# Performance work log

Hardware: AMD Instinct MI355X
Metric: run time of the kernel (lower is better)

Reference implementation:

```python
import jax, jax.numpy as jnp
import numpy as np

MAX_K_QK = 64
MAX_K_V = 64
MAX_K_KNOW = 128


def threshold_gate(scores, tau, max_k):
    # scores: [B,S,N], tau: [B,S,1]
    raw = scores - tau
    gate = jnp.where(raw > 0, raw, 1e-08 * jnp.exp(raw))
    exp_gate = jnp.exp(gate) - 1.0
    k = min(max_k, scores.shape[-1])
    topk_vals, _ = jax.lax.top_k(exp_gate, k)
    threshold = topk_vals[:, :, -1:]
    exp_gate = jnp.where(exp_gate >= threshold, exp_gate, 0.0)
    gate_sum = exp_gate.sum(axis=-1, keepdims=True) + 1e-08
    gate_strength = jnp.tanh(exp_gate.max(axis=-1, keepdims=True))
    return exp_gate / gate_sum * gate_strength


def setup_inputs() -> dict:
    key = jax.random.key(0)
    ks = jax.random.split(key, 8)
    B, S, D = 2, 2048, 1024
    N_QK, N_V, N_KNOW = 4096, 4096, 8192
    scale = 0.02  # keep scores in a sane range for exp()
    return {
        "x": jax.random.normal(ks[0], (B, S, D), jnp.float32),
        "qk_emb": jax.random.normal(ks[1], (N_QK, D), jnp.float32) * scale,
        "v_emb": jax.random.normal(ks[2], (N_V, D), jnp.float32) * scale,
        "know_emb": jax.random.normal(ks[3], (N_KNOW, D), jnp.float32) * scale,
        "w_attn": jax.random.normal(ks[4], (D, 3), jnp.float32) * scale,
        "b_attn": jnp.zeros((3,), jnp.float32),
        "w_know": jax.random.normal(ks[5], (D, 1), jnp.float32) * scale,
        "b_know": jnp.zeros((1,), jnp.float32),
    }


def reference(x, qk_emb, v_emb, know_emb, w_attn, b_attn, w_know, b_know):
    # deterministic=True -> router dropout is identity
    # attention gates
    scores_qk = jnp.einsum("bsd,nd->bsn", x, qk_emb)
    scores_v = jnp.einsum("bsd,nd->bsn", x, v_emb)
    tau_all = x @ w_attn + b_attn  # [B,S,3]
    g_Q = threshold_gate(scores_qk, tau_all[:, :, 0:1], MAX_K_QK)
    g_K = threshold_gate(scores_qk, tau_all[:, :, 1:2], MAX_K_QK)
    g_V = threshold_gate(scores_v, tau_all[:, :, 2:3], MAX_K_V)
    t_qk = 1.0 / qk_emb.shape[0]
    t_v = 1.0 / v_emb.shape[0]
    aux_attn = (
        ((g_Q.mean(axis=(0, 1)) - t_qk) ** 2).sum() * g_Q.shape[-1]
        + ((g_K.mean(axis=(0, 1)) - t_qk) ** 2).sum() * g_K.shape[-1]
        + ((g_V.mean(axis=(0, 1)) - t_v) ** 2).sum() * g_V.shape[-1]
    )
    # knowledge gates
    scores_know = jnp.einsum("bsd,nd->bsn", x, know_emb)
    tau_know = x @ w_know + b_know  # [B,S,1]
    g_know = threshold_gate(scores_know, tau_know, MAX_K_KNOW)
    t_know = 1.0 / know_emb.shape[0]
    aux_know = ((g_know.mean(axis=(0, 1)) - t_know) ** 2).sum() * g_know.shape[-1]
    return (g_Q, g_K, g_V, aux_attn, g_know, aux_know)
```

## Files before the change

### kernel.cpp

```cpp
#include <hip/hip_runtime.h>
#include <hip/hip_bf16.h>


#define M_ROWS 4096
#define DIM    1024
#define N_QK   4096
#define N_KNOW 8192

typedef unsigned short ushortT;
typedef __attribute__((ext_vector_type(8)))  short short8;
typedef __attribute__((ext_vector_type(16))) float f32x16;

__global__ __launch_bounds__(256) void tau_kernel(
    const float* __restrict__ x, const float* __restrict__ w_attn,
    const float* __restrict__ b_attn, const float* __restrict__ w_know,
    const float* __restrict__ b_know, float* __restrict__ tau4, int D)
{
    __shared__ float s_f[4][4];
    const int row = blockIdx.x;
    const int tid = threadIdx.x;
    const float* xr = x + (size_t)row * D;
    float p0 = 0.f, p1 = 0.f, p2 = 0.f, p3 = 0.f;
    for (int d = tid; d < D; d += 256) {
        float xv = xr[d];
        p0 += xv * w_attn[d * 3 + 0];
        p1 += xv * w_attn[d * 3 + 1];
        p2 += xv * w_attn[d * 3 + 2];
        p3 += xv * w_know[d];
    }
#pragma unroll
    for (int o = 32; o > 0; o >>= 1) {
        p0 += __shfl_down(p0, o, 64);
        p1 += __shfl_down(p1, o, 64);
        p2 += __shfl_down(p2, o, 64);
        p3 += __shfl_down(p3, o, 64);
    }
    const int lane = tid & 63, wv = tid >> 6;
    if (lane == 0) { s_f[wv][0] = p0; s_f[wv][1] = p1; s_f[wv][2] = p2; s_f[wv][3] = p3; }
    __syncthreads();
    if (tid < 4) {
        float v = s_f[0][tid] + s_f[1][tid] + s_f[2][tid] + s_f[3][tid];
        v += (tid < 3) ? b_attn[tid] : b_know[0];
        tau4[(size_t)row * 4 + tid] = v;
    }
}

__device__ __forceinline__ void split4(const float4 v, uint2& H, uint2& L) {
    float vv[4] = {v.x, v.y, v.z, v.w};
    unsigned h[4], l[4];
#pragma unroll
    for (int i = 0; i < 4; i++) {
        __hip_bfloat16 hb = __float2bfloat16(vv[i]);
        float r = vv[i] - __bfloat162float(hb);
        __hip_bfloat16 lb = __float2bfloat16(r);
        h[i] = *(ushortT*)&hb;
        l[i] = *(ushortT*)&lb;
    }
    H.x = h[0] | (h[1] << 16); H.y = h[2] | (h[3] << 16);
    L.x = l[0] | (l[1] << 16); L.y = l[2] | (l[3] << 16);
}

__global__ __launch_bounds__(256) void convertA(
    const float* __restrict__ src, ushortT* __restrict__ dst, int nElem4)
{
    int g = blockIdx.x * 256 + threadIdx.x;
    if (g >= nElem4) return;
    int row = g >> 8;
    int c4  = g & 255;
    int chunk = c4 >> 3, pos = c4 & 7;
    const float4 v = *(const float4*)(src + (size_t)row * DIM + c4 * 4);
    uint2 H, L;
    split4(v, H, L);
    ushortT* base = dst + (size_t)row * 2048 + chunk * 64;
    *(uint2*)(base + pos * 4)      = H;
    *(uint2*)(base + 32 + pos * 4) = L;
}

__global__ __launch_bounds__(256) void gemm_fused3(
    const ushortT* __restrict__ Aext, const ushortT* __restrict__ Bext,
    float* __restrict__ gQ, float* __restrict__ gV, float* __restrict__ gKn,
    int nb0)
{
    __shared__ ushortT AHL[2][128 * 64];
    __shared__ ushortT BHL[2][128 * 64];
    const int tid = threadIdx.x;
    const int wave = tid >> 6, lane = tid & 63;
    const int l32 = lane & 31, h = lane >> 5;
    const int rx7 = l32 & 7;
    const int wm = (wave >> 1) * 64, wn = (wave & 1) * 64;
    const long long m0 = (long long)blockIdx.y * 128;
    const int nblk = nb0 + blockIdx.x;

    float* C; long long ldc; long long n0;
    if (nblk < 32)      { C = gQ;  ldc = N_QK;   n0 = (long long)nblk * 128; }
    else if (nblk < 64) { C = gV;  ldc = N_QK;   n0 = (long long)(nblk - 32) * 128; }
    else                { C = gKn; ldc = N_KNOW; n0 = (long long)(nblk - 64) * 128; }

    const ushortT* gAp[4]; const ushortT* gBp[4]; int lOff[4];
#pragma unroll
    for (int it = 0; it < 4; ++it) {
        int f = it * 256 + tid;
        int r = f >> 3, sp = f & 7;
        int sg = sp ^ (r & 7);
        gAp[it] = Aext + (m0 + r) * 2048 + sg * 8;
        gBp[it] = Bext + ((long long)blockIdx.x * 128 + r) * 2048 + sg * 8;
        lOff[it] = f * 8;
    }

    f32x16 acc[2][2] = {};

#define STAGE(buf, c) do {                                                         \
    _Pragma("unroll")                                                              \
    for (int it = 0; it < 4; ++it) {                                               \
        __builtin_amdgcn_global_load_lds(                                          \
            (const __attribute__((address_space(1))) unsigned*)(const void*)(gAp[it] + (c) * 64), \
            (__attribute__((address_space(3))) unsigned*)(void*)(&AHL[buf][0] + lOff[it]), 16, 0, 0); \
        __builtin_amdgcn_global_load_lds(                                          \
            (const __attribute__((address_space(1))) unsigned*)(const void*)(gBp[it] + (c) * 64), \
            (__attribute__((address_space(3))) unsigned*)(void*)(&BHL[buf][0] + lOff[it]), 16, 0, 0); \
    }                                                                              \
} while (0)

#define COMPUTE(buf) do {                                                          \
    _Pragma("unroll")                                                              \
    for (int kb = 0; kb < 2; ++kb) {                                               \
        const int so = ((kb * 2 + h) ^ rx7) * 16;                                  \
        short8 aH[2], aL[2], bH[2], bL[2];                                         \
        _Pragma("unroll")                                                          \
        for (int t = 0; t < 2; ++t) {                                              \
            const char* pa = (const char*)(&AHL[buf][0]) + (wm + t * 32 + l32) * 128; \
            const char* pb = (const char*)(&BHL[buf][0]) + (wn + t * 32 + l32) * 128; \
            aH[t] = *(const short8*)(pa + so);                                     \
            aL[t] = *(const short8*)(pa + (so ^ 64));                              \
            bH[t] = *(const short8*)(pb + so);                                     \
            bL[t] = *(const short8*)(pb + (so ^ 64));                              \
        }                                                                          \
        _Pragma("unroll")                                                          \
        for (int i = 0; i < 2; ++i)                                                \
            _Pragma("unroll")                                                      \
            for (int j = 0; j < 2; ++j) {                                          \
                acc[i][j] = __builtin_amdgcn_mfma_f32_32x32x16_bf16(aH[i], bH[j], acc[i][j], 0, 0, 0); \
                acc[i][j] = __builtin_amdgcn_mfma_f32_32x32x16_bf16(aH[i], bL[j], acc[i][j], 0, 0, 0); \
                acc[i][j] = __builtin_amdgcn_mfma_f32_32x32x16_bf16(aL[i], bH[j], acc[i][j], 0, 0, 0); \
                acc[i][j] = __builtin_amdgcn_mfma_f32_32x32x16_bf16(aL[i], bL[j], acc[i][j], 0, 0, 0); \
            }                                                                      \
    }                                                                              \
} while (0)

    STAGE(0, 0);
    __syncthreads();

    for (int c = 0; c < 32; c += 2) {
        STAGE(1, c + 1);
        COMPUTE(0);
        __syncthreads();
        if (c + 2 < 32) STAGE(0, c + 2);
        COMPUTE(1);
        __syncthreads();
    }
#undef STAGE
#undef COMPUTE

#pragma unroll
    for (int ti = 0; ti < 2; ++ti)
#pragma unroll
        for (int tj = 0; tj < 2; ++tj) {
            long long col = n0 + wn + tj * 32 + l32;
            long long rb  = m0 + wm + ti * 32 + 4 * h;
#pragma unroll
            for (int reg = 0; reg < 16; ++reg) {
                long long row = rb + (reg & 3) + 8 * (reg >> 2);
                C[row * ldc + col] = acc[ti][tj][reg];
            }
        }
}

__global__ __launch_bounds__(256) void gemm_fused2(
    const ushortT* __restrict__ Aext, const float* __restrict__ qk_emb,
    const float* __restrict__ v_emb, const float* __restrict__ know_emb,
    float* __restrict__ gQ, float* __restrict__ gV, float* __restrict__ gKn,
    long long rowOff)
{
    __shared__ ushortT AHL[128 * 64];
    __shared__ ushortT BHL[128 * 64];
    const int tid = threadIdx.x;
    const int wave = tid >> 6, lane = tid & 63;
    const int l32 = lane & 31, h = lane >> 5;
    const int rx7 = l32 & 7;
    const int wm = (wave >> 1) * 64, wn = (wave & 1) * 64;
    const long long m0 = (long long)blockIdx.y * 128;
    const int nblk = blockIdx.x;

    const float* Bsrc; float* C; long long ldc; long long n0;
    if (nblk < 32)      { Bsrc = qk_emb;   C = gQ;  ldc = N_QK;   n0 = (long long)nblk * 128; }
    else if (nblk < 64) { Bsrc = v_emb;    C = gV;  ldc = N_QK;   n0 = (long long)(nblk - 32) * 128; }
    else                { Bsrc = know_emb; C = gKn; ldc = N_KNOW; n0 = (long long)(nblk - 64) * 128; }

    const ushortT* gAp[4]; ushortT* lAp[4];
    const float*   gBp[4]; int offH[4], offL[4];
#pragma unroll
    for (int it = 0; it < 4; ++it) {
        int f = it * 256 + tid;
        int r = f >> 3, sp = f & 7;
        int sg = sp ^ (r & 7);
        gAp[it] = Aext + (m0 + r) * 2048 + sg * 8;
        lAp[it] = AHL + f * 8;
        int c4 = f & 7;
        int s = c4 >> 1, hf = c4 & 1;
        offH[it] = r * 128 + ((s ^ (r & 7)) * 16) + hf * 8;
        offL[it] = r * 128 + (((4 | s) ^ (r & 7)) * 16) + hf * 8;
        gBp[it] = Bsrc + (n0 + r) * DIM + c4 * 4;
    }
    const char* pA[2]; const char* pB[2];
#pragma unroll
    for (int t = 0; t < 2; ++t) {
        pA[t] = (const char*)AHL + (wm + t * 32 + l32) * 128;
        pB[t] = (const char*)BHL + (wn + t * 32 + l32) * 128;
    }

    f32x16 acc[2][2] = {};
    float4 bufB[4];
#pragma unroll
    for (int it = 0; it < 4; ++it) bufB[it] = *(const float4*)(gBp[it]);

    for (int c = 0; c < 32; ++c) {
#pragma unroll
        for (int it = 0; it < 4; ++it) {
            __builtin_amdgcn_global_load_lds(
                (const __attribute__((address_space(1))) unsigned*)(const void*)(gAp[it] + c * 64),
                (__attribute__((address_space(3))) unsigned*)(void*)lAp[it], 16, 0, 0);
            uint2 H, L;
            split4(bufB[it], H, L);
            *(uint2*)((char*)BHL + offH[it]) = H;
            *(uint2*)((char*)BHL + offL[it]) = L;
        }
        __syncthreads();
        if (c + 1 < 32) {
#pragma unroll
            for (int it = 0; it < 4; ++it)
                bufB[it] = *(const float4*)(gBp[it] + (c + 1) * 32);
        }
#pragma unroll
        for (int kb = 0; kb < 2; ++kb) {
            const int so = ((kb * 2 + h) ^ rx7) * 16;
            short8 aH[2], aL[2], bH[2], bL[2];
#pragma unroll
            for (int t = 0; t < 2; ++t) {
                aH[t] = *(const short8*)(pA[t] + so);
                aL[t] = *(const short8*)(pA[t] + (so ^ 64));
                bH[t] = *(const short8*)(pB[t] + so);
                bL[t] = *(const short8*)(pB[t] + (so ^ 64));
            }
#pragma unroll
            for (int i = 0; i < 2; ++i)
#pragma unroll
                for (int j = 0; j < 2; ++j) {
                    acc[i][j] = __builtin_amdgcn_mfma_f32_32x32x16_bf16(aH[i], bH[j], acc[i][j], 0, 0, 0);
                    acc[i][j] = __builtin_amdgcn_mfma_f32_32x32x16_bf16(aH[i], bL[j], acc[i][j], 0, 0, 0);
                    acc[i][j] = __builtin_amdgcn_mfma_f32_32x32x16_bf16(aL[i], bH[j], acc[i][j], 0, 0, 0);
                    acc[i][j] = __builtin_amdgcn_mfma_f32_32x32x16_bf16(aL[i], bL[j], acc[i][j], 0, 0, 0);
                }
        }
        __syncthreads();
    }
#pragma unroll
    for (int ti = 0; ti < 2; ++ti)
#pragma unroll
        for (int tj = 0; tj < 2; ++tj) {
            long long col = n0 + wn + tj * 32 + l32;
            long long rb  = rowOff + m0 + wm + ti * 32 + 4 * h;
#pragma unroll
            for (int reg = 0; reg < 16; ++reg) {
                long long row = rb + (reg & 3) + 8 * (reg >> 2);
                C[row * ldc + col] = acc[ti][tj][reg];
            }
        }
}

__device__ __forceinline__ unsigned floatToKey(float f) {
    unsigned b = __float_as_uint(f);
    return (b & 0x80000000u) ? ~b : (b | 0x80000000u);
}
__device__ __forceinline__ float keyToFloat(unsigned key) {
    unsigned b = (key & 0x80000000u) ? (key & 0x7FFFFFFFu) : ~key;
    return __uint_as_float(b);
}
__device__ __forceinline__ float egate(float raw) {
    float g = raw > 0.f ? raw : 1e-8f * __expf(raw);
    return expf(g) - 1.f;
}

template <int NV, bool VLOAD, bool VSTORE>
__device__ __forceinline__ void gate_body(
    const float* __restrict__ srow, float tA, float tB, bool hasB, int ksel,
    float* __restrict__ orowA, float* __restrict__ orowB,
    float* __restrict__ colA, float* __restrict__ colB,
    int* s_cnt, unsigned* s_u, float* s_f)
{
    const int tid = threadIdx.x, lane = tid & 63, wv = tid >> 6;

    unsigned keys[NV * 4];
    unsigned kmax = 0u;
#pragma unroll
    for (int i = 0; i < NV; i++) {
        float v0, v1, v2, v3;
        if (VLOAD) {
            float4 v = *(const float4*)(srow + (size_t)(i * 256 + tid) * 4);
            v0 = v.x; v1 = v.y; v2 = v.z; v3 = v.w;
        } else {
            v0 = srow[(i * 4 + 0) * 256 + tid];
            v1 = srow[(i * 4 + 1) * 256 + tid];
            v2 = srow[(i * 4 + 2) * 256 + tid];
            v3 = srow[(i * 4 + 3) * 256 + tid];
        }
        unsigned a = floatToKey(v0), b = floatToKey(v1);
        unsigned c = floatToKey(v2), d = floatToKey(v3);
        keys[i * 4 + 0] = a; keys[i * 4 + 1] = b;
        keys[i * 4 + 2] = c; keys[i * 4 + 3] = d;
        unsigned m1 = a > b ? a : b, m2 = c > d ? c : d;
        m1 = m1 > m2 ? m1 : m2;
        kmax = kmax > m1 ? kmax : m1;
    }
#pragma unroll
    for (int o = 32; o > 0; o >>= 1) {
        unsigned x = __shfl_down(kmax, o, 64);
        kmax = kmax > x ? kmax : x;
    }
    if (lane == 0) s_u[wv] = kmax;
    __syncthreads();
    { unsigned a = s_u[0], b = s_u[1], c = s_u[2], d = s_u[3];
      unsigned m1 = a > b ? a : b, m2 = c > d ? c : d; kmax = m1 > m2 ? m1 : m2; }

    unsigned lo = 0u, hi = kmax, vk;
    int pp = 0;
    for (;;) {
        if (lo >= hi) { vk = lo; break; }
        unsigned mid = lo + ((hi - lo + 1u) >> 1);
        int c = 0;
#pragma unroll
        for (int i = 0; i < NV * 4; i++) c += (keys[i] >= mid) ? 1 : 0;
#pragma unroll
        for (int o = 32; o > 0; o >>= 1) c += __shfl_down(c, o, 64);
        if (lane == 0) s_cnt[pp * 4 + wv] = c;
        __syncthreads();
        int total = s_cnt[pp * 4 + 0] + s_cnt[pp * 4 + 1]
                  + s_cnt[pp * 4 + 2] + s_cnt[pp * 4 + 3];
        pp ^= 1;
        if (total == ksel) { vk = mid; break; }
        if (total > ksel) lo = mid; else hi = mid - 1u;
    }

    float sA = 0.f, sB = 0.f;
#pragma unroll
    for (int i = 0; i < NV * 4; i++) {
        if (keys[i] >= vk) {
            float s = keyToFloat(keys[i]);
            sA += egate(s - tA);
            if (hasB) sB += egate(s - tB);
        }
    }
#pragma unroll
    for (int o = 32; o > 0; o >>= 1) {
        sA += __shfl_down(sA, o, 64);
        sB += __shfl_down(sB, o, 64);
    }
    if (lane == 0) { s_f[wv] = sA; s_f[4 + wv] = sB; }
    __syncthreads();
    sA = s_f[0] + s_f[1] + s_f[2] + s_f[3];
    sB = s_f[4] + s_f[5] + s_f[6] + s_f[7];

    const float smax = keyToFloat(kmax);
    const float scaleA = tanhf(egate(smax - tA)) / (sA + 1e-8f);
    const float scaleB = hasB ? tanhf(egate(smax - tB)) / (sB + 1e-8f) : 0.f;

#pragma unroll
    for (int i = 0; i < NV; i++) {
        float ga[4], gb[4];
        int eidx[4];
#pragma unroll
        for (int j = 0; j < 4; j++) {
            int ii = i * 4 + j;
            int idx = VLOAD ? (i * 1024 + tid * 4 + j) : (ii * 256 + tid);
            eidx[j] = idx;
            unsigned key = keys[ii];
            float vA = 0.f, vB = 0.f;
            if (key >= vk) {
                float s = keyToFloat(key);
                vA = egate(s - tA) * scaleA;
                atomicAdd(&colA[idx], vA);
                if (hasB) { vB = egate(s - tB) * scaleB; atomicAdd(&colB[idx], vB); }
            }
            ga[j] = vA; gb[j] = vB;
        }
        if (VSTORE) {
            *(float4*)(orowA + (size_t)eidx[0]) = make_float4(ga[0], ga[1], ga[2], ga[3]);
            if (hasB) *(float4*)(orowB + (size_t)eidx[0]) = make_float4(gb[0], gb[1], gb[2], gb[3]);
        } else {
#pragma unroll
            for (int j = 0; j < 4; j++) {
                orowA[eidx[j]] = ga[j];
                if (hasB) orowB[eidx[j]] = gb[j];
            }
        }
    }
}

__global__ __launch_bounds__(256) void gate_all(
    const float* __restrict__ tau4,
    float* __restrict__ gQ, float* __restrict__ gK,
    float* __restrict__ gV, float* __restrict__ gKn,
    float* __restrict__ colsums)
{
    __shared__ int s_cnt[8];
    __shared__ unsigned s_u[4];
    __shared__ float s_f[8];
    const int bid = blockIdx.x;
    if (bid < 4096) {
        const int row = bid;
        const float t = tau4[(size_t)row * 4 + 3];
        gate_body<8, false, false>(
            gKn + (size_t)row * N_KNOW, t, 0.f, false, 128,
            gKn + (size_t)row * N_KNOW, nullptr,
            colsums + 3 * N_QK, nullptr, s_cnt, s_u, s_f);
    } else if (bid < 8192) {
        const int row = bid - 4096;
        const float tA = tau4[(size_t)row * 4 + 0];
        const float tB = tau4[(size_t)row * 4 + 1];
        gate_body<4, true, true>(
            gQ + (size_t)row * N_QK, tA, tB, true, 64,
            gQ + (size_t)row * N_QK, gK + (size_t)row * N_QK,
            colsums, colsums + N_QK, s_cnt, s_u, s_f);
    } else {
        const int row = bid - 8192;
        const float t = tau4[(size_t)row * 4 + 2];
        gate_body<4, true, true>(
            gV + (size_t)row * N_QK, t, 0.f, false, 64,
            gV + (size_t)row * N_QK, nullptr,
            colsums + 2 * N_QK, nullptr, s_cnt, s_u, s_f);
    }
}

__global__ __launch_bounds__(256) void aux_kernel(
    const float* __restrict__ colsum,
    float* __restrict__ auxAttn, float* __restrict__ auxKnow)
{
    __shared__ float s_a[4];
    __shared__ float s_b[4];
    const int tid = threadIdx.x;
    const int lane = tid & 63, wv = tid >> 6;
    const float invM = 1.f / 4096.f;

    float sa = 0.f;
    const float tqk = 1.f / 4096.f;
    for (int i = tid; i < 3 * N_QK; i += 256) {
        float m = colsum[i] * invM - tqk;
        sa += m * m;
    }
    float sk = 0.f;
    const float tkn = 1.f / 8192.f;
    for (int i = tid; i < N_KNOW; i += 256) {
        float m = colsum[3 * N_QK + i] * invM - tkn;
        sk += m * m;
    }
#pragma unroll
    for (int o = 32; o > 0; o >>= 1) {
        sa += __shfl_down(sa, o, 64);
        sk += __shfl_down(sk, o, 64);
    }
    if (lane == 0) { s_a[wv] = sa; s_b[wv] = sk; }
    __syncthreads();
    if (tid == 0) {
        auxAttn[0] = (s_a[0] + s_a[1] + s_a[2] + s_a[3]) * 4096.f;
        auxKnow[0] = (s_b[0] + s_b[1] + s_b[2] + s_b[3]) * 8192.f;
    }
}

static void convert_b_range(const float* qk, const float* v, const float* kn,
                            ushortT* Bext, long long rowLo, long long rowHi,
                            hipStream_t stream)
{
    struct Seg { const float* p; long long lo, hi; };
    Seg seg[3] = { {qk, 0, 4096}, {v, 4096, 8192}, {kn, 8192, 16384} };
    for (int i = 0; i < 3; ++i) {
        long long lo = rowLo > seg[i].lo ? rowLo : seg[i].lo;
        long long hi = rowHi < seg[i].hi ? rowHi : seg[i].hi;
        if (lo < hi) {
            int nel4 = (int)((hi - lo) * 256);
            convertA<<<(nel4 + 255) / 256, 256, 0, stream>>>(
                seg[i].p + (size_t)(lo - seg[i].lo) * DIM,
                Bext + (size_t)(lo - rowLo) * 2048, nel4);
        }
    }
}

extern "C" void kernel_launch(void* const* d_in, const int* in_sizes, int n_in,
                              void* d_out, int out_size, void* d_ws, size_t ws_size,
                              hipStream_t stream)
{
    const float* x        = (const float*)d_in[0];
    const float* qk_emb   = (const float*)d_in[1];
    const float* v_emb    = (const float*)d_in[2];
    const float* know_emb = (const float*)d_in[3];
    const float* w_attn   = (const float*)d_in[4];
    const float* b_attn   = (const float*)d_in[5];
    const float* w_know   = (const float*)d_in[6];
    const float* b_know   = (const float*)d_in[7];
    float* out = (float*)d_out;

    const long long M = M_ROWS;

    float* gQ   = out;
    float* gK   = gQ + (size_t)M * N_QK;
    float* gV   = gK + (size_t)M * N_QK;
    float* auxA = gV + (size_t)M * N_QK;
    float* gKn  = auxA + 1;
    float* auxK = gKn + (size_t)M * N_KNOW;

    const long long nColsum = 3 * N_QK + N_KNOW;
    const long long tail_bytes = (M * 4 + nColsum) * 4;
    long long tailStart = ((long long)ws_size - tail_bytes) & ~255LL;
    float* tau4 = (float*)((char*)d_ws + tailStart);
    float* colsums = tau4 + (size_t)M * 4;

    const long long rowB = 4096;
    const long long aBytes = M * rowB;

    hipMemsetAsync(colsums, 0, nColsum * sizeof(float), stream);
    tau_kernel<<<(int)M, 256, 0, stream>>>(x, w_attn, b_attn, w_know, b_know, tau4, DIM);

    long long availB = tailStart - aBytes;
    long long nbc = availB > 0 ? availB / (128 * rowB) : 0;
    if (nbc > 128) nbc = 128;

    if (nbc >= 32) {
        ushortT* A_ext = (ushortT*)d_ws;
        ushortT* B_ext = (ushortT*)((char*)d_ws + aBytes);
        convertA<<<(int)(M * 256 / 256), 256, 0, stream>>>(x, A_ext, (int)(M * 256));
        for (long long nb0 = 0; nb0 < 128; nb0 += nbc) {
            long long nn = (128 - nb0 < nbc) ? (128 - nb0) : nbc;
            convert_b_range(qk_emb, v_emb, know_emb, B_ext,
                            nb0 * 128, (nb0 + nn) * 128, stream);
            gemm_fused3<<<dim3((unsigned)nn, 32), 256, 0, stream>>>(
                A_ext, B_ext, gQ, gV, gKn, (int)nb0);
        }
    } else {
        long long ra = (tailStart / rowB / 128) * 128;
        if (ra > M) ra = M;
        if (ra < 128) ra = 128;
        ushortT* A_ext = (ushortT*)d_ws;
        for (long long a0 = 0; a0 < M; a0 += ra) {
            long long ac = (M - a0 < ra) ? (M - a0) : ra;
            int nel4 = (int)(ac * 256);
            convertA<<<(nel4 + 255) / 256, 256, 0, stream>>>(x + a0 * DIM, A_ext, nel4);
            gemm_fused2<<<dim3(128, (unsigned)(ac / 128)), 256, 0, stream>>>(
                A_ext, qk_emb, v_emb, know_emb, gQ, gV, gKn, a0);
        }
    }

    gate_all<<<12288, 256, 0, stream>>>(tau4, gQ, gK, gV, gKn, colsums);

    aux_kernel<<<1, 256, 0, stream>>>(colsums, auxA, auxK);
}
```

Measured before the change: 1.053 ms.

## Replace binary-search top-k threshold with 4-pass radix select; reorder MFMA chain

```diff
diff --git a/kernel.cpp b/kernel.cpp
--- a/kernel.cpp
+++ b/kernel.cpp
@@ -138,12 +138,23 @@
         _Pragma("unroll")                                                          \
         for (int i = 0; i < 2; ++i)                                                \
             _Pragma("unroll")                                                      \
-            for (int j = 0; j < 2; ++j) {                                          \
+            for (int j = 0; j < 2; ++j)                                            \
                 acc[i][j] = __builtin_amdgcn_mfma_f32_32x32x16_bf16(aH[i], bH[j], acc[i][j], 0, 0, 0); \
+        _Pragma("unroll")                                                          \
+        for (int i = 0; i < 2; ++i)                                                \
+            _Pragma("unroll")                                                      \
+            for (int j = 0; j < 2; ++j)                                            \
                 acc[i][j] = __builtin_amdgcn_mfma_f32_32x32x16_bf16(aH[i], bL[j], acc[i][j], 0, 0, 0); \
+        _Pragma("unroll")                                                          \
+        for (int i = 0; i < 2; ++i)                                                \
+            _Pragma("unroll")                                                      \
+            for (int j = 0; j < 2; ++j)                                            \
                 acc[i][j] = __builtin_amdgcn_mfma_f32_32x32x16_bf16(aL[i], bH[j], acc[i][j], 0, 0, 0); \
+        _Pragma("unroll")                                                          \
+        for (int i = 0; i < 2; ++i)                                                \
+            _Pragma("unroll")                                                      \
+            for (int j = 0; j < 2; ++j)                                            \
                 acc[i][j] = __builtin_amdgcn_mfma_f32_32x32x16_bf16(aL[i], bL[j], acc[i][j], 0, 0, 0); \
-            }                                                                      \
     }                                                                              \
 } while (0)
 
@@ -295,7 +306,7 @@
     const float* __restrict__ srow, float tA, float tB, bool hasB, int ksel,
     float* __restrict__ orowA, float* __restrict__ orowB,
     float* __restrict__ colA, float* __restrict__ colB,
-    int* s_cnt, unsigned* s_u, float* s_f)
+    int* s_hist, unsigned* s_u, float* s_f)
 {
     const int tid = threadIdx.x, lane = tid & 63, wv = tid >> 6;
 
@@ -330,25 +341,49 @@
     __syncthreads();
     { unsigned a = s_u[0], b = s_u[1], c = s_u[2], d = s_u[3];
       unsigned m1 = a > b ? a : b, m2 = c > d ? c : d; kmax = m1 > m2 ? m1 : m2; }
-
-    unsigned lo = 0u, hi = kmax, vk;
-    int pp = 0;
-    for (;;) {
-        if (lo >= hi) { vk = lo; break; }
-        unsigned mid = lo + ((hi - lo + 1u) >> 1);
-        int c = 0;
-#pragma unroll
-        for (int i = 0; i < NV * 4; i++) c += (keys[i] >= mid) ? 1 : 0;
-#pragma unroll
-        for (int o = 32; o > 0; o >>= 1) c += __shfl_down(c, o, 64);
-        if (lane == 0) s_cnt[pp * 4 + wv] = c;
-        __syncthreads();
-        int total = s_cnt[pp * 4 + 0] + s_cnt[pp * 4 + 1]
-                  + s_cnt[pp * 4 + 2] + s_cnt[pp * 4 + 3];
-        pp ^= 1;
-        if (total == ksel) { vk = mid; break; }
-        if (total > ksel) lo = mid; else hi = mid - 1u;
-    }
+    __syncthreads();
+
+    unsigned prefix = 0u;
+    int kk = ksel;
+#pragma unroll
+    for (int rnd = 0; rnd < 4; ++rnd) {
+        const int sh = 24 - 8 * rnd;
+        s_hist[tid] = 0;
+        __syncthreads();
+#pragma unroll
+        for (int i = 0; i < NV * 4; i++) {
+            unsigned key = keys[i];
+            if ((((key ^ prefix) >> sh) >> 8) == 0u)
+                atomicAdd(&s_hist[(key >> sh) & 255u], 1);
+        }
+        __syncthreads();
+        if (tid < 64) {
+            const int b3 = 255 - 4 * tid;
+            const int h0 = s_hist[b3],     h1 = s_hist[b3 - 1];
+            const int h2 = s_hist[b3 - 2], h3 = s_hist[b3 - 3];
+            const int gsum = h0 + h1 + h2 + h3;
+            int inc = gsum;
+#pragma unroll
+            for (int o = 1; o < 64; o <<= 1) {
+                int v = __shfl_up(inc, o, 64);
+                if (tid >= o) inc += v;
+            }
+            const int above = inc - gsum;
+            const int c0 = above + h0, c1 = c0 + h1, c2 = c1 + h2, c3 = c2 + h3;
+            if (kk > above && kk <= c3) {
+                unsigned byt; int nk;
+                if (kk <= c0)      { byt = (unsigned)b3;       nk = kk - above; }
+                else if (kk <= c1) { byt = (unsigned)(b3 - 1); nk = kk - c0; }
+                else if (kk <= c2) { byt = (unsigned)(b3 - 2); nk = kk - c1; }
+                else               { byt = (unsigned)(b3 - 3); nk = kk - c2; }
+                s_u[0] = byt; s_u[1] = (unsigned)nk;
+            }
+        }
+        __syncthreads();
+        prefix |= s_u[0] << sh;
+        kk = (int)s_u[1];
+    }
+    const unsigned vk = prefix;
 
     float sA = 0.f, sB = 0.f;
 #pragma unroll
@@ -411,7 +446,7 @@
     float* __restrict__ gV, float* __restrict__ gKn,
     float* __restrict__ colsums)
 {
-    __shared__ int s_cnt[8];
+    __shared__ int s_hist[256];
     __shared__ unsigned s_u[4];
     __shared__ float s_f[8];
     const int bid = blockIdx.x;
@@ -421,7 +456,7 @@
         gate_body<8, false, false>(
             gKn + (size_t)row * N_KNOW, t, 0.f, false, 128,
             gKn + (size_t)row * N_KNOW, nullptr,
-            colsums + 3 * N_QK, nullptr, s_cnt, s_u, s_f);
+            colsums + 3 * N_QK, nullptr, s_hist, s_u, s_f);
     } else if (bid < 8192) {
         const int row = bid - 4096;
         const float tA = tau4[(size_t)row * 4 + 0];
@@ -429,14 +464,14 @@
         gate_body<4, true, true>(
             gQ + (size_t)row * N_QK, tA, tB, true, 64,
             gQ + (size_t)row * N_QK, gK + (size_t)row * N_QK,
-            colsums, colsums + N_QK, s_cnt, s_u, s_f);
+            colsums, colsums + N_QK, s_hist, s_u, s_f);
     } else {
         const int row = bid - 8192;
         const float t = tau4[(size_t)row * 4 + 2];
         gate_body<4, true, true>(
             gV + (size_t)row * N_QK, t, 0.f, false, 64,
             gV + (size_t)row * N_QK, nullptr,
-            colsums + 2 * N_QK, nullptr, s_cnt, s_u, s_f);
+            colsums + 2 * N_QK, nullptr, s_hist, s_u, s_f);
     }
 }
 
```

After: 1.058 ms. No clear change (+0.5%).
